# Performance work log

Measured on AMD Instinct MI355X. Metric: run time of the kernel, lower is better.

## Reference

```python
import jax, jax.numpy as jnp
import numpy as np

REL_SIZE = 65
TAG_SIZE = 4


def _rope(y):
    # Interleaved rotary position embedding, matching the torch module:
    # cos_pos = cos(theta) repeat_interleave(2), sin_pos = sin(theta) repeat_interleave(2)
    # y2 = (-y1, y0, -y3, y2, ...)
    B, S, H = y.shape
    half = H // 2
    pos = jnp.arange(S, dtype=jnp.float32)[:, None]                      # (S,1)
    inv_freq = jnp.power(10000.0, -2.0 * jnp.arange(half, dtype=jnp.float32) / H)
    theta = pos * inv_freq                                               # (S, half)
    cos = jnp.repeat(jnp.cos(theta), 2, axis=-1)                          # (S, H)
    sin = jnp.repeat(jnp.sin(theta), 2, axis=-1)                          # (S, H)
    yr = y.reshape(B, S, half, 2)
    y2 = jnp.stack([-yr[..., 1], yr[..., 0]], axis=-1).reshape(B, S, H)
    return y * cos + y2 * sin


def setup_inputs() -> dict:
    key = jax.random.key(0)
    k1, k2, k3 = jax.random.split(key, 3)
    B, S, H = 1, 160, 768
    y = jax.random.normal(k1, (B, S, H), dtype=jnp.float32)
    event_idx = jax.random.randint(k2, (B, 16), 0, S)
    W1 = jax.random.normal(k3, (H, 2 * H), dtype=jnp.float32) * 0.02
    b1 = jnp.zeros((H,), dtype=jnp.float32)
    W2 = jax.random.normal(jax.random.fold_in(key, 7), (REL_SIZE * TAG_SIZE, H), dtype=jnp.float32) * 0.02
    b2 = jnp.zeros((REL_SIZE * TAG_SIZE,), dtype=jnp.float32)
    return {"y": y, "event_idx": event_idx, "W1": W1, "b1": b1, "W2": W2, "b2": b2}


def reference(y, event_idx, W1, b1, W2, b2):
    # Eval path (training=False): event_idx unused, dropout = identity, sigmoid applied.
    B, S, H = y.shape
    yrot = _rope(y)
    # Linear(cat(a, b)) is separable: split W1 into the halves acting on a and b.
    Wa, Wb = W1[:, :H], W1[:, H:]
    left = jnp.einsum('bsh,oh->bso', yrot, Wa)                  # contribution of token i (row)
    right = jnp.einsum('bsh,oh->bso', yrot, Wb) + b1            # contribution of token j (col)
    h = jax.nn.relu(left[:, :, None, :] + right[:, None, :, :])  # (B, S, S, H)
    out = jnp.einsum('bijh,oh->bijo', h, W2) + b2               # (B, S, S, 260)
    out = out.reshape(B, S, S, REL_SIZE, TAG_SIZE).transpose(0, 3, 1, 2, 4)  # (B, 65, S, S, 4)
    return jax.nn.sigmoid(out)
```

## Files before the change

### kernel.cpp

```cpp
#include <hip/hip_runtime.h>
#include <hip/hip_bf16.h>
#include <cstdint>

#define SDIM 160
#define HDIM 768
#define HALF 384
#define ODIM 260
#define OPAD 272
#define CHUNK_BYTES 34816
#define WS_SMALL 1155088
#define WS_BIG   3514384

typedef __attribute__((ext_vector_type(8))) short short8;
typedef __attribute__((ext_vector_type(4))) float floatx4;
typedef _Float16 half8 __attribute__((ext_vector_type(8)));

typedef const __attribute__((address_space(1))) unsigned char gl_u8;
typedef __attribute__((address_space(3))) unsigned char lds_u8;

static __device__ __forceinline__ float bf2f(unsigned short u) {
    union { unsigned int i; float f; } v; v.i = ((unsigned int)u) << 16; return v.f;
}
static __device__ __forceinline__ unsigned short f2bf(float x) {
    __hip_bfloat16 h = __float2bfloat16(x);
    return *reinterpret_cast<unsigned short*>(&h);
}
static __device__ __forceinline__ unsigned short f2h(float x) {
    _Float16 h = (_Float16)x;
    return *reinterpret_cast<unsigned short*>(&h);
}
static __device__ __forceinline__ float q(float x) { return bf2f(f2bf(x)); }

__global__ __launch_bounds__(256) void prep_kernel(
    const float* __restrict__ y, const float* __restrict__ W1,
    const float* __restrict__ W2,
    unsigned short* __restrict__ yb, unsigned short* __restrict__ W2b,
    unsigned short* __restrict__ W1b, int do_w1b) {
    int bid = blockIdx.x;
    int t = threadIdx.x;
    if (bid < SDIM) {
        int s = bid;
        for (int p = t; p < HALF; p += 256) {
            float invf = __expf(-(2.0f * (float)p / (float)HDIM) * 9.210340371976184f);
            float th = (float)s * invf;
            float c = cosf(th), sn = sinf(th);
            float y0 = y[s * HDIM + 2 * p], y1 = y[s * HDIM + 2 * p + 1];
            yb[s * HDIM + 2 * p]     = f2bf(y0 * c - y1 * sn);
            yb[s * HDIM + 2 * p + 1] = f2bf(y1 * c + y0 * sn);
        }
    } else if (bid < SDIM + 102) {
        int idx = (bid - SDIM) * 256 + t;
        if (idx < 96 * OPAD) {
            int kg = idx % 96, row = idx / 96;
            unsigned short o8[8];
            if (row < ODIM) {
                float4 a = *reinterpret_cast<const float4*>(W2 + row * HDIM + kg * 8);
                float4 b = *reinterpret_cast<const float4*>(W2 + row * HDIM + kg * 8 + 4);
                o8[0] = f2h(a.x); o8[1] = f2h(a.y); o8[2] = f2h(a.z); o8[3] = f2h(a.w);
                o8[4] = f2h(b.x); o8[5] = f2h(b.y); o8[6] = f2h(b.z); o8[7] = f2h(b.w);
            } else {
                #pragma unroll
                for (int e = 0; e < 8; ++e) o8[e] = 0;
            }
            *reinterpret_cast<uint4*>(W2b + ((size_t)kg * OPAD + row) * 8) =
                *reinterpret_cast<uint4*>(o8);
        }
    } else if (do_w1b) {
        int idx = (bid - SDIM - 102) * 256 + t;
        int kg = idx % 96, row = idx / 96;
        const float* src = (row < 768) ? (W1 + row * 1536 + kg * 8)
                                       : (W1 + (row - 768) * 1536 + 768 + kg * 8);
        float4 a = *reinterpret_cast<const float4*>(src);
        float4 b = *reinterpret_cast<const float4*>(src + 4);
        unsigned short o8[8];
        o8[0] = f2bf(a.x); o8[1] = f2bf(a.y); o8[2] = f2bf(a.z); o8[3] = f2bf(a.w);
        o8[4] = f2bf(b.x); o8[5] = f2bf(b.y); o8[6] = f2bf(b.z); o8[7] = f2bf(b.w);
        *reinterpret_cast<uint4*>(W1b + ((size_t)kg * 1536 + row) * 8) =
            *reinterpret_cast<uint4*>(o8);
    }
}

__global__ __launch_bounds__(64, 2) void lr3_kernel(
    const unsigned short* __restrict__ yb, const unsigned short* __restrict__ W1b,
    const float* __restrict__ b1,
    unsigned short* __restrict__ Lb, unsigned short* __restrict__ Rt) {
    int l = threadIdx.x & 63;
    int l16 = l & 15, qd = l >> 4;
    int mtb = blockIdx.x * 4;
    int sp = blockIdx.y;
    int s0 = sp * 32 + l16;
    int s1 = s0 + 16;

    floatx4 acc[2][4];
    #pragma unroll
    for (int st = 0; st < 2; ++st)
        #pragma unroll
        for (int mtl = 0; mtl < 4; ++mtl)
            acc[st][mtl] = (floatx4){0.0f, 0.0f, 0.0f, 0.0f};

    const unsigned short* yrow0 = yb + s0 * HDIM;
    const unsigned short* yrow1 = yb + s1 * HDIM;

    for (int ks = 0; ks < 24; ++ks) {
        int k = ks * 32 + qd * 8;
        int kg = ks * 4 + qd;
        union { uint4 u; short8 s; } bu0, bu1;
        bu0.u = *reinterpret_cast<const uint4*>(yrow0 + k);
        bu1.u = *reinterpret_cast<const uint4*>(yrow1 + k);
        #pragma unroll
        for (int mtl = 0; mtl < 4; ++mtl) {
            union { uint4 u; short8 s; } au;
            au.u = *reinterpret_cast<const uint4*>(
                W1b + ((size_t)kg * 1536 + (mtb + mtl) * 16 + l16) * 8);
            acc[0][mtl] = __builtin_amdgcn_mfma_f32_16x16x32_bf16(
                au.s, bu0.s, acc[0][mtl], 0, 0, 0);
            acc[1][mtl] = __builtin_amdgcn_mfma_f32_16x16x32_bf16(
                au.s, bu1.s, acc[1][mtl], 0, 0, 0);
        }
    }

    #pragma unroll
    for (int st = 0; st < 2; ++st) {
        int s_out = sp * 32 + st * 16 + l16;
        #pragma unroll
        for (int mtl = 0; mtl < 4; ++mtl) {
            int o2 = (mtb + mtl) * 16 + qd * 4;
            unsigned short out4[4];
            if (o2 < 768) {
                #pragma unroll
                for (int r = 0; r < 4; ++r) out4[r] = f2h(acc[st][mtl][r]);
                *reinterpret_cast<uint2*>(Lb + s_out * HDIM + o2) =
                    *reinterpret_cast<uint2*>(out4);
            } else {
                int ob = o2 - 768;
                #pragma unroll
                for (int r = 0; r < 4; ++r)
                    out4[r] = f2h(acc[st][mtl][r] + b1[ob + r]);
                *reinterpret_cast<uint2*>(
                    Rt + ((size_t)(ob >> 3) * SDIM + s_out) * 8 + (ob & 7)) =
                    *reinterpret_cast<uint2*>(out4);
            }
        }
    }
}

__global__ __launch_bounds__(256) void lr_fallback_kernel(
    const unsigned short* __restrict__ yb, const float* __restrict__ W1,
    const float* __restrict__ b1,
    unsigned short* __restrict__ Lb, unsigned short* __restrict__ Rt) {
    int idx = blockIdx.x * 256 + threadIdx.x;
    int s = idx / 1536;
    int o2 = idx - s * 1536;
    const unsigned short* yrow = yb + s * HDIM;
    if (o2 < 768) {
        const float* wp = W1 + o2 * 1536;
        float a0 = 0.0f;
        for (int k = 0; k < HDIM; ++k) a0 += q(wp[k]) * bf2f(yrow[k]);
        Lb[s * HDIM + o2] = f2h(a0);
    } else {
        int ob = o2 - 768;
        const float* wp = W1 + ob * 1536 + 768;
        float a0 = 0.0f;
        for (int k = 0; k < HDIM; ++k) a0 += q(wp[k]) * bf2f(yrow[k]);
        Rt[((size_t)(ob >> 3) * SDIM + s) * 8 + (ob & 7)] = f2h(a0 + b1[ob]);
    }
}

__global__ __launch_bounds__(512) void main_kernel(
    const unsigned short* __restrict__ Lb, const unsigned short* __restrict__ Rt,
    const unsigned short* __restrict__ W2b,
    const float* __restrict__ b2, float* __restrict__ out) {
    __shared__ __align__(16) unsigned char lds[2 * CHUNK_BYTES];

    int w = threadIdx.x >> 6;
    int l = threadIdx.x & 63;
    int l16 = l & 15, qd = l >> 4;
    int jh = w & 1;
    int mq = w >> 1;
    int mt0 = mq * 4;
    int nmt = (mq == 3) ? 5 : 4;
    int i0 = blockIdx.x * 2;
    int j = blockIdx.y * 32 + jh * 16 + l16;

    floatx4 acc[2][5];
    #pragma unroll
    for (int c = 0; c < 2; ++c)
        #pragma unroll
        for (int mtl = 0; mtl < 5; ++mtl)
            acc[c][mtl] = (floatx4){0.0f, 0.0f, 0.0f, 0.0f};

    const unsigned short* Lrow0 = Lb + i0 * HDIM;
    const unsigned short* Lrow1 = Lb + (i0 + 1) * HDIM;
    const unsigned char* wsrc = reinterpret_cast<const unsigned char*>(W2b);

    #pragma unroll
    for (int it = 0; it < 5; ++it) {
        int seg = w + it * 8;
        if (seg < 34) {
            __builtin_amdgcn_global_load_lds(
                (gl_u8*)(wsrc + seg * 1024 + l * 16),
                (lds_u8*)(lds + seg * 1024), 16, 0, 0);
        }
    }
    __syncthreads();

    for (int kc = 0; kc < 12; ++kc) {
        int buf = kc & 1;
        if (kc < 11) {
            const unsigned char* gsrc = wsrc + (kc + 1) * CHUNK_BYTES;
            unsigned char* ldst = lds + (1 - buf) * CHUNK_BYTES;
            #pragma unroll
            for (int it = 0; it < 5; ++it) {
                int seg = w + it * 8;
                if (seg < 34) {
                    __builtin_amdgcn_global_load_lds(
                        (gl_u8*)(gsrc + seg * 1024 + l * 16),
                        (lds_u8*)(ldst + seg * 1024), 16, 0, 0);
                }
            }
        }
        #pragma unroll
        for (int ks = 0; ks < 2; ++ks) {
            int k = kc * 64 + ks * 32 + qd * 8;
            int kg = kc * 8 + ks * 4 + qd;
            half8 bfrag[2];
            union { uint4 u; half8 h; } ru;
            ru.u = *reinterpret_cast<const uint4*>(
                Rt + ((size_t)kg * SDIM + j) * 8);
            #pragma unroll
            for (int c = 0; c < 2; ++c) {
                const unsigned short* Lr = c ? Lrow1 : Lrow0;
                union { uint4 u; half8 h; } lu;
                lu.u = *reinterpret_cast<const uint4*>(Lr + k);
                half8 hv = lu.h + ru.h;
                #pragma unroll
                for (int e = 0; e < 8; ++e)
                    hv[e] = hv[e] > (_Float16)0.0f ? hv[e] : (_Float16)0.0f;
                bfrag[c] = hv;
            }
            int ldsbase = buf * CHUNK_BYTES + ((ks * 4 + qd) * OPAD + l16) * 16;
            #pragma unroll
            for (int mtl = 0; mtl < 5; ++mtl) {
                if (mtl < nmt) {
                    union { uint4 u; half8 h; } au;
                    au.u = *reinterpret_cast<const uint4*>(
                        lds + ldsbase + (mt0 + mtl) * 256);
                    acc[0][mtl] = __builtin_amdgcn_mfma_f32_16x16x32_f16(
                        au.h, bfrag[0], acc[0][mtl], 0, 0, 0);
                    acc[1][mtl] = __builtin_amdgcn_mfma_f32_16x16x32_f16(
                        au.h, bfrag[1], acc[1][mtl], 0, 0, 0);
                }
            }
        }
        __syncthreads();
    }

    #pragma unroll
    for (int c = 0; c < 2; ++c) {
        int i = i0 + c;
        #pragma unroll
        for (int mtl = 0; mtl < 5; ++mtl) {
            if (mtl < nmt) {
                int ob = (mt0 + mtl) * 16 + qd * 4;
                if (ob < ODIM) {
                    float4 bv = *reinterpret_cast<const float4*>(b2 + ob);
                    int rel = ob >> 2;
                    float4 v;
                    v.x = 1.0f / (1.0f + __expf(-(acc[c][mtl][0] + bv.x)));
                    v.y = 1.0f / (1.0f + __expf(-(acc[c][mtl][1] + bv.y)));
                    v.z = 1.0f / (1.0f + __expf(-(acc[c][mtl][2] + bv.z)));
                    v.w = 1.0f / (1.0f + __expf(-(acc[c][mtl][3] + bv.w)));
                    *reinterpret_cast<float4*>(
                        out + (((rel * SDIM) + i) * SDIM + j) * 4) = v;
                }
            }
        }
    }
}

__global__ void ws_too_small_kernel(float* out) { out[0] = 999.0f; }

extern "C" void kernel_launch(void* const* d_in, const int* in_sizes, int n_in,
                              void* d_out, int out_size, void* d_ws, size_t ws_size,
                              hipStream_t stream) {
    const float* y  = (const float*)d_in[0];
    const float* W1 = (const float*)d_in[2];
    const float* b1 = (const float*)d_in[3];
    const float* W2 = (const float*)d_in[4];
    const float* b2 = (const float*)d_in[5];
    float* out = (float*)d_out;

    if (ws_size < (size_t)WS_SMALL) {
        ws_too_small_kernel<<<dim3(1), dim3(1), 0, stream>>>(out);
        return;
    }

    unsigned short* yb  = (unsigned short*)((char*)d_ws + 16);
    unsigned short* Lb  = yb + SDIM * HDIM;
    unsigned short* Rt  = Lb + SDIM * HDIM;
    unsigned short* W2b = Rt + SDIM * HDIM;
    unsigned short* W1b = W2b + 96 * OPAD * 8;

    if (ws_size >= (size_t)WS_BIG) {
        prep_kernel<<<dim3(SDIM + 102 + 576), dim3(256), 0, stream>>>(
            y, W1, W2, yb, W2b, W1b, 1);
        lr3_kernel<<<dim3(24, 5), dim3(64), 0, stream>>>(yb, W1b, b1, Lb, Rt);
        main_kernel<<<dim3(80, 5), dim3(512), 0, stream>>>(Lb, Rt, W2b, b2, out);
    } else {
        prep_kernel<<<dim3(SDIM + 102), dim3(256), 0, stream>>>(
            y, W1, W2, yb, W2b, W1b, 0);
        lr_fallback_kernel<<<dim3(960), dim3(256), 0, stream>>>(yb, W1, b1, Lb, Rt);
        main_kernel<<<dim3(80, 5), dim3(512), 0, stream>>>(Lb, Rt, W2b, b2, out);
    }
}
```

Before: 118.3 us.

## Split W2 output rows into two halves across a new grid dimension

The main kernel's 272 padded output rows are split into two halves (144 and 128 rows), and the grid gets a z dimension of 2 so each block handles one half. W2b is re-laid out in the prep kernel as two contiguous half-blocks so each block streams only its half into LDS. This halves LDS use and per-wave accumulators, which should raise occupancy and double the block count. In exchange, the ReLU(L+R) B-fragment computation and the Rt/L loads are duplicated across the two halves.

```diff
diff --git a/kernel.cpp b/kernel.cpp
--- a/kernel.cpp
+++ b/kernel.cpp
@@ -7,7 +7,9 @@
 #define HALF 384
 #define ODIM 260
 #define OPAD 272
-#define CHUNK_BYTES 34816
+#define H0_ROWS 144
+#define H1_ROWS 128
+#define H0_BYTES 18432
 #define WS_SMALL 1155088
 #define WS_BIG   3514384
 
@@ -62,7 +64,10 @@
                 #pragma unroll
                 for (int e = 0; e < 8; ++e) o8[e] = 0;
             }
-            *reinterpret_cast<uint4*>(W2b + ((size_t)kg * OPAD + row) * 8) =
+            size_t dst = (row < H0_ROWS)
+                ? ((size_t)kg * H0_ROWS + row)
+                : ((size_t)96 * H0_ROWS + (size_t)kg * H1_ROWS + (row - H0_ROWS));
+            *reinterpret_cast<uint4*>(W2b + dst * 8) =
                 *reinterpret_cast<uint4*>(o8);
         }
     } else if (do_w1b) {
@@ -170,35 +175,41 @@
     const unsigned short* __restrict__ Lb, const unsigned short* __restrict__ Rt,
     const unsigned short* __restrict__ W2b,
     const float* __restrict__ b2, float* __restrict__ out) {
-    __shared__ __align__(16) unsigned char lds[2 * CHUNK_BYTES];
+    __shared__ __align__(16) unsigned char lds[2 * H0_BYTES];
 
     int w = threadIdx.x >> 6;
     int l = threadIdx.x & 63;
     int l16 = l & 15, qd = l >> 4;
     int jh = w & 1;
     int mq = w >> 1;
-    int mt0 = mq * 4;
-    int nmt = (mq == 3) ? 5 : 4;
+    int h = blockIdx.z;
+    int nrows = h ? H1_ROWS : H0_ROWS;
+    int hb = nrows * 128;
+    int nseg = nrows >> 3;
+    int mt0l = mq * 2;
+    int nmt = (h == 0 && mq == 3) ? 3 : 2;
+    int mtg0 = h * 9;
     int i0 = blockIdx.x * 2;
     int j = blockIdx.y * 32 + jh * 16 + l16;
 
-    floatx4 acc[2][5];
+    floatx4 acc[2][3];
     #pragma unroll
     for (int c = 0; c < 2; ++c)
         #pragma unroll
-        for (int mtl = 0; mtl < 5; ++mtl)
+        for (int mtl = 0; mtl < 3; ++mtl)
             acc[c][mtl] = (floatx4){0.0f, 0.0f, 0.0f, 0.0f};
 
     const unsigned short* Lrow0 = Lb + i0 * HDIM;
     const unsigned short* Lrow1 = Lb + (i0 + 1) * HDIM;
-    const unsigned char* wsrc = reinterpret_cast<const unsigned char*>(W2b);
-
-    #pragma unroll
-    for (int it = 0; it < 5; ++it) {
+    const unsigned char* wbase = reinterpret_cast<const unsigned char*>(W2b)
+        + (h ? (size_t)96 * H0_ROWS * 16 : 0);
+
+    #pragma unroll
+    for (int it = 0; it < 3; ++it) {
         int seg = w + it * 8;
-        if (seg < 34) {
+        if (seg < nseg) {
             __builtin_amdgcn_global_load_lds(
-                (gl_u8*)(wsrc + seg * 1024 + l * 16),
+                (gl_u8*)(wbase + seg * 1024 + l * 16),
                 (lds_u8*)(lds + seg * 1024), 16, 0, 0);
         }
     }
@@ -207,12 +218,12 @@
     for (int kc = 0; kc < 12; ++kc) {
         int buf = kc & 1;
         if (kc < 11) {
-            const unsigned char* gsrc = wsrc + (kc + 1) * CHUNK_BYTES;
-            unsigned char* ldst = lds + (1 - buf) * CHUNK_BYTES;
+            const unsigned char* gsrc = wbase + (size_t)(kc + 1) * hb;
+            unsigned char* ldst = lds + (1 - buf) * hb;
             #pragma unroll
-            for (int it = 0; it < 5; ++it) {
+            for (int it = 0; it < 3; ++it) {
                 int seg = w + it * 8;
-                if (seg < 34) {
+                if (seg < nseg) {
                     __builtin_amdgcn_global_load_lds(
                         (gl_u8*)(gsrc + seg * 1024 + l * 16),
                         (lds_u8*)(ldst + seg * 1024), 16, 0, 0);
@@ -238,13 +249,13 @@
                     hv[e] = hv[e] > (_Float16)0.0f ? hv[e] : (_Float16)0.0f;
                 bfrag[c] = hv;
             }
-            int ldsbase = buf * CHUNK_BYTES + ((ks * 4 + qd) * OPAD + l16) * 16;
+            int ldsbase = buf * hb + ((ks * 4 + qd) * nrows + mt0l * 16 + l16) * 16;
             #pragma unroll
-            for (int mtl = 0; mtl < 5; ++mtl) {
+            for (int mtl = 0; mtl < 3; ++mtl) {
                 if (mtl < nmt) {
                     union { uint4 u; half8 h; } au;
                     au.u = *reinterpret_cast<const uint4*>(
-                        lds + ldsbase + (mt0 + mtl) * 256);
+                        lds + ldsbase + mtl * 256);
                     acc[0][mtl] = __builtin_amdgcn_mfma_f32_16x16x32_f16(
                         au.h, bfrag[0], acc[0][mtl], 0, 0, 0);
                     acc[1][mtl] = __builtin_amdgcn_mfma_f32_16x16x32_f16(
@@ -259,9 +270,9 @@
     for (int c = 0; c < 2; ++c) {
         int i = i0 + c;
         #pragma unroll
-        for (int mtl = 0; mtl < 5; ++mtl) {
+        for (int mtl = 0; mtl < 3; ++mtl) {
             if (mtl < nmt) {
-                int ob = (mt0 + mtl) * 16 + qd * 4;
+                int ob = (mtg0 + mt0l + mtl) * 16 + qd * 4;
                 if (ob < ODIM) {
                     float4 bv = *reinterpret_cast<const float4*>(b2 + ob);
                     int rel = ob >> 2;
@@ -305,11 +316,11 @@
         prep_kernel<<<dim3(SDIM + 102 + 576), dim3(256), 0, stream>>>(
             y, W1, W2, yb, W2b, W1b, 1);
         lr3_kernel<<<dim3(24, 5), dim3(64), 0, stream>>>(yb, W1b, b1, Lb, Rt);
-        main_kernel<<<dim3(80, 5), dim3(512), 0, stream>>>(Lb, Rt, W2b, b2, out);
+        main_kernel<<<dim3(80, 5, 2), dim3(512), 0, stream>>>(Lb, Rt, W2b, b2, out);
     } else {
         prep_kernel<<<dim3(SDIM + 102), dim3(256), 0, stream>>>(
             y, W1, W2, yb, W2b, W1b, 0);
         lr_fallback_kernel<<<dim3(960), dim3(256), 0, stream>>>(yb, W1, b1, Lb, Rt);
-        main_kernel<<<dim3(80, 5), dim3(512), 0, stream>>>(Lb, Rt, W2b, b2, out);
-    }
-}
+        main_kernel<<<dim3(80, 5, 2), dim3(512), 0, stream>>>(Lb, Rt, W2b, b2, out);
+    }
+}
```

Measured after the change: 125.2 us. 1.06x slower.
